# Optimization experiments

Hardware: AMD Instinct MI355X
Metric: run time of the kernel (lower is better)

## Reference

```python
import jax, jax.numpy as jnp
import numpy as np

MARGIN = 0.3
B, D = 512, 128
NUM_CLASSES = 64


def setup_inputs() -> dict:
    key = jax.random.key(0)
    k1, k2 = jax.random.split(key)
    emb = jax.random.normal(k1, (B, D), dtype=jnp.float32)
    emb = emb / jnp.linalg.norm(emb, axis=-1, keepdims=True)  # docstring: L2-normalized
    labels = jax.random.randint(k2, (B,), 0, NUM_CLASSES, dtype=jnp.int64)
    return {"embeddings": emb, "labels": labels}


def reference(embeddings, labels):
    b = embeddings.shape[0]
    # pairwise euclidean distances (torch.cdist p=2)
    sq = jnp.sum(embeddings * embeddings, axis=-1)
    d2 = sq[:, None] + sq[None, :] - 2.0 * (embeddings @ embeddings.T)
    dist = jnp.sqrt(jnp.maximum(d2, 1e-12))  # [B, B]

    eq = labels[:, None] == labels[None, :]
    eye = jnp.eye(b, dtype=bool)
    pos_mask = eq & ~eye          # [i, p]
    neg_mask = ~eq                # [i, j]

    NEG_BIG = jnp.float32(-1e30)
    POS_BIG = jnp.float32(1e30)

    d_ap = dist[:, :, None]       # [i, p, 1]
    d_an = dist[:, None, :]       # [i, 1, j]
    # semi-hard: negative farther than positive but within margin
    semi = neg_mask[:, None, :] & (d_an > d_ap) & (d_an < d_ap + MARGIN)  # [i, p, j]
    semi_max = jnp.max(jnp.where(semi, d_an, NEG_BIG), axis=2)            # [i, p]
    has_semi = jnp.any(semi, axis=2)                                      # [i, p]
    # fallback: hardest (closest) negative per anchor
    min_neg = jnp.min(jnp.where(neg_mask, dist, POS_BIG), axis=1)         # [i]
    d_neg = jnp.where(has_semi, semi_max, min_neg[:, None])               # [i, p]

    has_neg = jnp.any(neg_mask, axis=1)
    valid = pos_mask & has_neg[:, None]

    per_pair = jax.nn.relu(dist - d_neg + MARGIN)
    total = jnp.sum(jnp.where(valid, per_pair, 0.0))
    cnt = jnp.sum(valid)
    return jnp.where(cnt > 0, total / jnp.maximum(cnt, 1).astype(total.dtype), jnp.float32(0.0))
```

## Files before the change

### kernel.cpp

```cpp
#include <hip/hip_runtime.h>

#define BN 512
#define DIM 128
#define TMARGIN 0.3f
#define NT 512
#define NW 8
#define NBLK 256

#define FMA4(ACC, U, V)                                                \
    ACC.x += U.x * V.x; ACC.y += U.y * V.y;                            \
    ACC.z += U.z * V.z; ACC.w += U.w * V.w;

__device__ __forceinline__ float hsum4(float4 v) {
    return (v.x + v.y) + (v.z + v.w);
}

__global__ __launch_bounds__(NT, 1) void triplet_fused_kernel(
        const float* __restrict__ emb,
        const int* __restrict__ labels,
        float* __restrict__ psum,
        float* __restrict__ pcnt) {
    const int ia   = blockIdx.x;
    const int ib   = blockIdx.x + 256;
    const int tid  = threadIdx.x;
    const int lane = tid & 63;
    const int wave = tid >> 6;

    __shared__ float4 ea4[DIM / 4], eb4[DIM / 4];
    __shared__ float  drowA[BN], drowB[BN];
    __shared__ int    lab[BN];
    __shared__ int    posA[BN], posB[BN];
    __shared__ int    nposA, nposB;
    __shared__ float  wsum[NW];
    __shared__ int    wcnt[NW];

    const float4* emb4 = (const float4*)emb;

    if (tid < 32)                 ea4[tid]      = emb4[(size_t)ia * 32 + tid];
    else if (tid < 64)            eb4[tid - 32] = emb4[(size_t)ib * 32 + (tid - 32)];
    lab[tid] = labels[tid];
    if (tid == 0) { nposA = 0; nposB = 0; }
    __syncthreads();

    float4 sva = {0,0,0,0}, svb = {0,0,0,0};
#pragma unroll
    for (int q = 0; q < DIM / 4; ++q) {
        float4 ua = ea4[q]; FMA4(sva, ua, ua);
        float4 ub = eb4[q]; FMA4(svb, ub, ub);
    }
    const float sqA = hsum4(sva);
    const float sqB = hsum4(svb);

    const int rl = lane >> 2;
    const int kl = lane & 3;
#pragma unroll
    for (int c = 0; c < 4; ++c) {
        const int r = c * 128 + wave * 16 + rl;
        float4 da = {0,0,0,0}, db = {0,0,0,0}, qq = {0,0,0,0};
#pragma unroll
        for (int q = 0; q < 8; ++q) {
            const int k4 = kl + 4 * q;
            const float4 v  = emb4[(size_t)r * 32 + k4];
            const float4 ua = ea4[k4];
            const float4 ub = eb4[k4];
            FMA4(da, ua, v);
            FMA4(db, ub, v);
            FMA4(qq, v, v);
        }
        float dotA = hsum4(da), dotB = hsum4(db), sqj = hsum4(qq);
        dotA += __shfl_down(dotA, 1); dotA += __shfl_down(dotA, 2);
        dotB += __shfl_down(dotB, 1); dotB += __shfl_down(dotB, 2);
        sqj  += __shfl_down(sqj, 1);  sqj  += __shfl_down(sqj, 2);
        if (kl == 0) {
            drowA[r] = sqrtf(fmaxf(sqA + sqj - 2.f * dotA, 1e-12f));
            drowB[r] = sqrtf(fmaxf(sqB + sqj - 2.f * dotB, 1e-12f));
        }
    }

    {
        const int grp = tid >> 8;
        const int t   = tid & 255;
        const int li  = grp ? lab[ib] : lab[ia];
        const int self = grp ? ib : ia;
        int* plist = grp ? posB : posA;
        int* pn    = grp ? &nposB : &nposA;
        for (int j = t; j < BN; j += 256) {
            if (lab[j] == li && j != self) {
                int p = atomicAdd(pn, 1);
                plist[p] = j;
            }
        }
    }
    __syncthreads();

    const int grp   = wave >> 2;
    const int wsub  = wave & 3;
    const float* drow = grp ? drowB : drowA;
    const int*  plist = grp ? posB  : posA;
    const int   npos  = grp ? nposB : nposA;
    const int   li    = grp ? lab[ib] : lab[ia];

    float mn = 1e30f;
    int   hn = 0;
    for (int k = lane; k < BN; k += 64) {
        if (lab[k] != li) { hn = 1; mn = fminf(mn, drow[k]); }
    }
#pragma unroll
    for (int off = 32; off > 0; off >>= 1) {
        mn = fminf(mn, __shfl_down(mn, off));
        hn |= __shfl_down(hn, off);
    }
    mn = __shfl(mn, 0);
    hn = __shfl(hn, 0);

    float lsum = 0.f;
    int   lcnt = 0;
    if (hn) {
        for (int p = wsub; p < npos; p += 4) {
            const float dap = drow[plist[p]];
            const float hi  = dap + TMARGIN;
            float smax = -1e30f;
            for (int k = lane; k < BN; k += 64) {
                const float dan = drow[k];
                if (lab[k] != li && dan > dap && dan < hi)
                    smax = fmaxf(smax, dan);
            }
#pragma unroll
            for (int off = 32; off > 0; off >>= 1)
                smax = fmaxf(smax, __shfl_down(smax, off));
            if (lane == 0) {
                const float dneg = (smax > -1e29f) ? smax : mn;
                lsum += fmaxf(dap - dneg + TMARGIN, 0.f);
                lcnt += 1;
            }
        }
    }
    if (lane == 0) { wsum[wave] = lsum; wcnt[wave] = lcnt; }
    __syncthreads();

    if (tid == 0) {
        float s = 0.f;
        int   c = 0;
#pragma unroll
        for (int w = 0; w < NW; ++w) { s += wsum[w]; c += wcnt[w]; }
        psum[blockIdx.x] = s;
        pcnt[blockIdx.x] = (float)c;
    }
}

__global__ __launch_bounds__(256) void finalize_kernel(
        const float* __restrict__ psum,
        const float* __restrict__ pcnt,
        float* __restrict__ out) {
    const int tid  = threadIdx.x;
    const int lane = tid & 63;
    const int wave = tid >> 6;
    __shared__ float ws_[4], wc_[4];

    float s = psum[tid];
    float c = pcnt[tid];
#pragma unroll
    for (int off = 32; off > 0; off >>= 1) {
        s += __shfl_down(s, off);
        c += __shfl_down(c, off);
    }
    if (lane == 0) { ws_[wave] = s; wc_[wave] = c; }
    __syncthreads();
    if (tid == 0) {
        float total = ws_[0] + ws_[1] + ws_[2] + ws_[3];
        float cnt   = wc_[0] + wc_[1] + wc_[2] + wc_[3];
        out[0] = (cnt > 0.f) ? (total / fmaxf(cnt, 1.f)) : 0.f;
    }
}

extern "C" void kernel_launch(void* const* d_in, const int* in_sizes, int n_in,
                              void* d_out, int out_size, void* d_ws, size_t ws_size,
                              hipStream_t stream) {
    const float* emb    = (const float*)d_in[0];
    const int*   labels = (const int*)d_in[1];
    float*       out    = (float*)d_out;
    float*       psum   = (float*)d_ws;
    float*       pcnt   = psum + NBLK;

    triplet_fused_kernel<<<NBLK, NT, 0, stream>>>(emb, labels, psum, pcnt);
    finalize_kernel<<<1, 256, 0, stream>>>(psum, pcnt, out);
}
```

Before: 70.74 us.

## Mask same-label distances inline and store positive distances directly, dropping label staging

```diff
diff --git a/kernel.cpp b/kernel.cpp
--- a/kernel.cpp
+++ b/kernel.cpp
@@ -6,6 +6,7 @@
 #define NT 512
 #define NW 8
 #define NBLK 256
+#define BIGF 1e30f
 
 #define FMA4(ACC, U, V)                                                \
     ACC.x += U.x * V.x; ACC.y += U.y * V.y;                            \
@@ -21,50 +22,48 @@
         float* __restrict__ psum,
         float* __restrict__ pcnt) {
     const int ia   = blockIdx.x;
-    const int ib   = blockIdx.x + 256;
+    const int ib   = blockIdx.x + NBLK;
     const int tid  = threadIdx.x;
     const int lane = tid & 63;
     const int wave = tid >> 6;
+    const int rl   = lane >> 2;
+    const int kl   = lane & 3;
 
-    __shared__ float4 ea4[DIM / 4], eb4[DIM / 4];
-    __shared__ float  drowA[BN], drowB[BN];
-    __shared__ int    lab[BN];
-    __shared__ int    posA[BN], posB[BN];
-    __shared__ int    nposA, nposB;
-    __shared__ float  wsum[NW];
-    __shared__ int    wcnt[NW];
+    __shared__ float drowA[BN], drowB[BN];
+    __shared__ float pdA[BN], pdB[BN];
+    __shared__ int   nposA, nposB;
+    __shared__ float wsum[NW];
+    __shared__ int   wcnt[NW];
 
     const float4* emb4 = (const float4*)emb;
+    const int liA = labels[ia];
+    const int liB = labels[ib];
 
-    if (tid < 32)                 ea4[tid]      = emb4[(size_t)ia * 32 + tid];
-    else if (tid < 64)            eb4[tid - 32] = emb4[(size_t)ib * 32 + (tid - 32)];
-    lab[tid] = labels[tid];
+    float4 ra[8], rb[8];
+#pragma unroll
+    for (int q = 0; q < 8; ++q) {
+        ra[q] = emb4[(size_t)ia * 32 + kl + 4 * q];
+        rb[q] = emb4[(size_t)ib * 32 + kl + 4 * q];
+    }
+    float4 sa = {0,0,0,0}, sb = {0,0,0,0};
+#pragma unroll
+    for (int q = 0; q < 8; ++q) { FMA4(sa, ra[q], ra[q]); FMA4(sb, rb[q], rb[q]); }
+    float sqA = hsum4(sa), sqB = hsum4(sb);
+    sqA += __shfl_xor(sqA, 1); sqA += __shfl_xor(sqA, 2);
+    sqB += __shfl_xor(sqB, 1); sqB += __shfl_xor(sqB, 2);
+
     if (tid == 0) { nposA = 0; nposB = 0; }
     __syncthreads();
 
-    float4 sva = {0,0,0,0}, svb = {0,0,0,0};
-#pragma unroll
-    for (int q = 0; q < DIM / 4; ++q) {
-        float4 ua = ea4[q]; FMA4(sva, ua, ua);
-        float4 ub = eb4[q]; FMA4(svb, ub, ub);
-    }
-    const float sqA = hsum4(sva);
-    const float sqB = hsum4(svb);
-
-    const int rl = lane >> 2;
-    const int kl = lane & 3;
 #pragma unroll
     for (int c = 0; c < 4; ++c) {
         const int r = c * 128 + wave * 16 + rl;
         float4 da = {0,0,0,0}, db = {0,0,0,0}, qq = {0,0,0,0};
 #pragma unroll
         for (int q = 0; q < 8; ++q) {
-            const int k4 = kl + 4 * q;
-            const float4 v  = emb4[(size_t)r * 32 + k4];
-            const float4 ua = ea4[k4];
-            const float4 ub = eb4[k4];
-            FMA4(da, ua, v);
-            FMA4(db, ub, v);
+            const float4 v = emb4[(size_t)r * 32 + kl + 4 * q];
+            FMA4(da, ra[q], v);
+            FMA4(db, rb[q], v);
             FMA4(qq, v, v);
         }
         float dotA = hsum4(da), dotB = hsum4(db), sqj = hsum4(qq);
@@ -72,67 +71,50 @@
         dotB += __shfl_down(dotB, 1); dotB += __shfl_down(dotB, 2);
         sqj  += __shfl_down(sqj, 1);  sqj  += __shfl_down(sqj, 2);
         if (kl == 0) {
-            drowA[r] = sqrtf(fmaxf(sqA + sqj - 2.f * dotA, 1e-12f));
-            drowB[r] = sqrtf(fmaxf(sqB + sqj - 2.f * dotB, 1e-12f));
-        }
-    }
-
-    {
-        const int grp = tid >> 8;
-        const int t   = tid & 255;
-        const int li  = grp ? lab[ib] : lab[ia];
-        const int self = grp ? ib : ia;
-        int* plist = grp ? posB : posA;
-        int* pn    = grp ? &nposB : &nposA;
-        for (int j = t; j < BN; j += 256) {
-            if (lab[j] == li && j != self) {
-                int p = atomicAdd(pn, 1);
-                plist[p] = j;
-            }
+            const int   lr = labels[r];
+            const float dA = sqrtf(fmaxf(sqA + sqj - 2.f * dotA, 1e-12f));
+            const float dB = sqrtf(fmaxf(sqB + sqj - 2.f * dotB, 1e-12f));
+            const bool  eqA = (lr == liA), eqB = (lr == liB);
+            drowA[r] = eqA ? BIGF : dA;
+            drowB[r] = eqB ? BIGF : dB;
+            if (eqA && r != ia) { int p = atomicAdd(&nposA, 1); pdA[p] = dA; }
+            if (eqB && r != ib) { int p = atomicAdd(&nposB, 1); pdB[p] = dB; }
         }
     }
     __syncthreads();
 
-    const int grp   = wave >> 2;
-    const int wsub  = wave & 3;
+    const int grp  = wave >> 2;
+    const int wsub = wave & 3;
     const float* drow = grp ? drowB : drowA;
-    const int*  plist = grp ? posB  : posA;
-    const int   npos  = grp ? nposB : nposA;
-    const int   li    = grp ? lab[ib] : lab[ia];
+    const float* pd   = grp ? pdB   : pdA;
+    const int    npos = grp ? nposB : nposA;
 
-    float mn = 1e30f;
-    int   hn = 0;
-    for (int k = lane; k < BN; k += 64) {
-        if (lab[k] != li) { hn = 1; mn = fminf(mn, drow[k]); }
-    }
+    float mn = BIGF;
 #pragma unroll
-    for (int off = 32; off > 0; off >>= 1) {
-        mn = fminf(mn, __shfl_down(mn, off));
-        hn |= __shfl_down(hn, off);
-    }
-    mn = __shfl(mn, 0);
-    hn = __shfl(hn, 0);
+    for (int kk = 0; kk < BN / 64; ++kk)
+        mn = fminf(mn, drow[lane + 64 * kk]);
+#pragma unroll
+    for (int off = 32; off; off >>= 1)
+        mn = fminf(mn, __shfl_xor(mn, off));
 
     float lsum = 0.f;
     int   lcnt = 0;
-    if (hn) {
+    if (mn < 1e29f) {
         for (int p = wsub; p < npos; p += 4) {
-            const float dap = drow[plist[p]];
+            const float dap = pd[p];
             const float hi  = dap + TMARGIN;
-            float smax = -1e30f;
-            for (int k = lane; k < BN; k += 64) {
-                const float dan = drow[k];
-                if (lab[k] != li && dan > dap && dan < hi)
-                    smax = fmaxf(smax, dan);
+            float smax = -BIGF;
+#pragma unroll
+            for (int kk = 0; kk < BN / 64; ++kk) {
+                const float dan = drow[lane + 64 * kk];
+                if (dan > dap && dan < hi) smax = fmaxf(smax, dan);
             }
 #pragma unroll
-            for (int off = 32; off > 0; off >>= 1)
-                smax = fmaxf(smax, __shfl_down(smax, off));
-            if (lane == 0) {
-                const float dneg = (smax > -1e29f) ? smax : mn;
-                lsum += fmaxf(dap - dneg + TMARGIN, 0.f);
-                lcnt += 1;
-            }
+            for (int off = 32; off; off >>= 1)
+                smax = fmaxf(smax, __shfl_xor(smax, off));
+            const float dneg = (smax > -1e29f) ? smax : mn;
+            lsum += fmaxf(dap - dneg + TMARGIN, 0.f);
+            lcnt += 1;
         }
     }
     if (lane == 0) { wsum[wave] = lsum; wcnt[wave] = lcnt; }
@@ -148,29 +130,24 @@
     }
 }
 
-__global__ __launch_bounds__(256) void finalize_kernel(
+__global__ __launch_bounds__(64) void finalize_kernel(
         const float* __restrict__ psum,
         const float* __restrict__ pcnt,
         float* __restrict__ out) {
-    const int tid  = threadIdx.x;
-    const int lane = tid & 63;
-    const int wave = tid >> 6;
-    __shared__ float ws_[4], wc_[4];
-
-    float s = psum[tid];
-    float c = pcnt[tid];
+    const int lane = threadIdx.x;
+    float s = 0.f, c = 0.f;
 #pragma unroll
-    for (int off = 32; off > 0; off >>= 1) {
-        s += __shfl_down(s, off);
-        c += __shfl_down(c, off);
+    for (int i = 0; i < 4; ++i) {
+        s += psum[lane + 64 * i];
+        c += pcnt[lane + 64 * i];
     }
-    if (lane == 0) { ws_[wave] = s; wc_[wave] = c; }
-    __syncthreads();
-    if (tid == 0) {
-        float total = ws_[0] + ws_[1] + ws_[2] + ws_[3];
-        float cnt   = wc_[0] + wc_[1] + wc_[2] + wc_[3];
-        out[0] = (cnt > 0.f) ? (total / fmaxf(cnt, 1.f)) : 0.f;
+#pragma unroll
+    for (int off = 32; off; off >>= 1) {
+        s += __shfl_xor(s, off);
+        c += __shfl_xor(c, off);
     }
+    if (lane == 0)
+        out[0] = (c > 0.f) ? (s / fmaxf(c, 1.f)) : 0.f;
 }
 
 extern "C" void kernel_launch(void* const* d_in, const int* in_sizes, int n_in,
@@ -183,5 +160,5 @@
     float*       pcnt   = psum + NBLK;
 
     triplet_fused_kernel<<<NBLK, NT, 0, stream>>>(emb, labels, psum, pcnt);
-    finalize_kernel<<<1, 256, 0, stream>>>(psum, pcnt, out);
+    finalize_kernel<<<1, 64, 0, stream>>>(psum, pcnt, out);
 }
```

Result: faster. 66.22 us (-6.4%).
